# Kernel optimization log

Hardware: AMD Instinct MI355X
Metric: run time of the kernel (lower is better)

The kernel has to match this reference:

```python
import jax, jax.numpy as jnp
import numpy as np

EPS = 1e-5

def _bn(x, g, b, axes):
    # training-mode BatchNorm: biased batch stats over `axes`
    mu = jnp.mean(x, axis=axes, keepdims=True)
    var = jnp.var(x, axis=axes, keepdims=True)
    return (x - mu) * jax.lax.rsqrt(var + EPS) * g + b

def setup_inputs() -> dict:
    key = jax.random.key(0)
    ks = jax.random.split(key, 8)
    N, C, T, V = 32, 64, 512, 25
    H, D, BC = 3, 8, 16
    return {
        'x': jax.random.normal(ks[0], (N, C, T, V), jnp.float32),
        'A_topo': jax.random.uniform(ks[1], (H, V, V), jnp.float32),
        'ln_g': jnp.ones((C,), jnp.float32),
        'ln_b': jnp.zeros((C,), jnp.float32),
        'qk_w': jax.random.normal(ks[2], (2 * H * D, C), jnp.float32),
        'qk_b': jnp.zeros((2 * H * D,), jnp.float32),
        'convd_w': jax.random.normal(ks[3], (H, C, C), jnp.float32) * 0.05,
        'convd_b': jnp.zeros((H, C), jnp.float32),
        'sagc_bn_g': jnp.ones((C,), jnp.float32),
        'sagc_bn_b': jnp.zeros((C,), jnp.float32),
        'tcn_w1': jax.random.normal(ks[4], (4, BC, C), jnp.float32) * 0.1,
        'tcn_b1': jnp.zeros((4, BC), jnp.float32),
        'tcn_bn1_g': jnp.ones((4, BC), jnp.float32),
        'tcn_bn1_b': jnp.zeros((4, BC), jnp.float32),
        'tcn_w2': jax.random.normal(ks[5], (2, BC, BC, 5), jnp.float32) * 0.1,
        'tcn_b2': jnp.zeros((2, BC), jnp.float32),
        'tcn_bn2_g': jnp.ones((3, BC), jnp.float32),
        'tcn_bn2_b': jnp.zeros((3, BC), jnp.float32),
    }

def reference(x, A_topo, ln_g, ln_b, qk_w, qk_b, convd_w, convd_b,
              sagc_bn_g, sagc_bn_b, tcn_w1, tcn_b1, tcn_bn1_g, tcn_bn1_b,
              tcn_w2, tcn_b2, tcn_bn2_g, tcn_bn2_b):
    N, C, T, V = x.shape
    H = A_topo.shape[0]
    D = qk_w.shape[0] // (2 * H)
    scale = D ** -0.5

    # ---- SelfAttention ----
    feat = jnp.transpose(x, (0, 2, 3, 1))              # n t v c
    mu = feat.mean(-1, keepdims=True)
    var = feat.var(-1, keepdims=True)
    y = (feat - mu) * jax.lax.rsqrt(var + EPS) * ln_g + ln_b
    qk = y @ qk_w.T + qk_b                             # n t v 2HD
    q, k = jnp.split(qk, 2, axis=-1)
    q = q.reshape(N, T, V, H, D)
    k = k.reshape(N, T, V, H, D)
    dots = jnp.einsum('ntihd,ntjhd->nthij', q, k) * scale
    attn = jax.nn.softmax(dots, axis=-1)               # n t h v v

    # ---- SA_GC ----
    A = attn * A_topo                                  # broadcast (H,V,V)
    z = jnp.einsum('nthij,ntjc->nthic', A, feat)       # per-head A_h @ feature
    sa = jnp.einsum('nthic,hoc->noti', z, convd_w)     # fused per-head 1x1 convs
    sa = sa + convd_b.sum(0)[None, :, None, None]
    sa = _bn(sa, sagc_bn_g[None, :, None, None], sagc_bn_b[None, :, None, None], (0, 2, 3))
    y_gc = jax.nn.relu(sa + x)                         # down = identity (in==out)

    # ---- MultiScale_TemporalConv ----
    pre = jnp.einsum('nctv,koc->nkotv', y_gc, tcn_w1) + tcn_b1[None, :, :, None, None]
    pre = _bn(pre, tcn_bn1_g[None, :, :, None, None], tcn_bn1_b[None, :, :, None, None], (0, 3, 4))
    act = jax.nn.relu(pre[:, :3])                      # branches 0..2 get ReLU
    branches = []
    for i, d in enumerate((1, 2)):                     # dilated temporal convs
        pad = 2 * d                                    # (kernel-1)*d//2
        w = tcn_w2[i][:, :, :, None]                   # (O,I,5,1)
        zb = jax.lax.conv_general_dilated(
            act[:, i], w, (1, 1), ((pad, pad), (0, 0)), rhs_dilation=(d, 1),
            dimension_numbers=('NCHW', 'OIHW', 'NCHW'))
        zb = zb + tcn_b2[i][None, :, None, None]
        zb = _bn(zb, tcn_bn2_g[i][None, :, None, None], tcn_bn2_b[i][None, :, None, None], (0, 2, 3))
        branches.append(zb)
    p = jax.lax.reduce_window(act[:, 2], -jnp.inf, jax.lax.max,
                              (1, 1, 3, 1), (1, 1, 1, 1),
                              ((0, 0), (0, 0), (1, 1), (0, 0)))
    p = _bn(p, tcn_bn2_g[2][None, :, None, None], tcn_bn2_b[2][None, :, None, None], (0, 2, 3))
    branches.append(p)
    branches.append(pre[:, 3])                         # plain 1x1 branch
    tcn_out = jnp.concatenate(branches, axis=1)        # (N, C, T, V)

    # ---- EncodingBlock residual (identity: in==out, stride==1) ----
    return jax.nn.relu(tcn_out + x)
```

## Files before the change

### kernel.cpp

```cpp
#include <hip/hip_runtime.h>


#define EPS 1e-5f

typedef __bf16 bf16;
typedef __bf16 bf16x8 __attribute__((ext_vector_type(8)));
typedef float f32x4 __attribute__((ext_vector_type(4)));

__global__ void kprepack(const float* __restrict__ qk_w, const float* __restrict__ convd_w,
                         const float* __restrict__ w1g,
                         bf16* __restrict__ qkB, bf16* __restrict__ convB, bf16* __restrict__ w1B)
{
  int gid = blockIdx.x * 256 + threadIdx.x;
  if (gid < 384) {
    int lane = gid & 63, f = gid >> 6;
    int nt = f >> 1, ks = f & 1;
    int row = nt * 16 + (lane & 15);
    int col = ks * 32 + ((lane >> 4) * 8);
    const float* src = &qk_w[row * 64 + col];
    bf16* dh = &qkB[(f * 64 + lane) * 8];
    bf16* dl = dh + 3072;
    #pragma unroll
    for (int j = 0; j < 8; j++) {
      float w = src[j];
      bf16 h = (bf16)w;
      dh[j] = h;
      dl[j] = (bf16)(w - (float)h);
    }
  } else if (gid < 1920) {
    int g = gid - 384;
    int lane = g & 63, f = g >> 6;
    int nt = f / 6, ks = f - nt * 6;
    int k0 = ks * 32 + ((lane >> 4) * 8);
    int h = k0 >> 6, c = k0 & 63;
    int o = nt * 16 + (lane & 15);
    const float* src = &convd_w[(h * 64 + o) * 64 + c];
    bf16* d = &convB[(f * 64 + lane) * 8];
    #pragma unroll
    for (int j = 0; j < 8; j++) d[j] = (bf16)src[j];
  } else if (gid < 2432) {
    int g = gid - 1920;
    int lane = g & 63, f = g >> 6;
    int nt = f >> 1, ks = f & 1;
    int ko = nt * 16 + (lane & 15);
    int c0 = ks * 32 + ((lane >> 4) * 8);
    const float* src = &w1g[ko * 64 + c0];
    bf16* dh = &w1B[(f * 64 + lane) * 8];
    bf16* dl = dh + 4096;
    #pragma unroll
    for (int j = 0; j < 8; j++) {
      float w = src[j];
      bf16 h = (bf16)w;
      dh[j] = h;
      dl[j] = (bf16)(w - (float)h);
    }
  }
}

__global__ __launch_bounds__(256, 5)
void k1_sa_sagc(const float* __restrict__ x,
                const float* __restrict__ topo,
                const float* __restrict__ ln_g, const float* __restrict__ ln_b,
                const float* __restrict__ qk_b,
                const bf16* __restrict__ qkB, const bf16* __restrict__ convB,
                const float* __restrict__ convd_b,
                bf16* __restrict__ saB, float* __restrict__ pSum, float* __restrict__ pSq)
{
  const int t = blockIdx.x, n = blockIdx.y, tid = threadIdx.x;
  const int blk = n * 512 + t;
  const int lane = tid & 63, wave = tid >> 6;
  const int rr = lane & 15, co = (lane >> 4) * 8, rq = (lane >> 4) * 4;

  __shared__ __align__(16) float smem[7928];
  bf16*  featT  = (bf16*)smem;
  bf16*  yH     = (bf16*)(smem + 1280);
  bf16*  yL     = (bf16*)(smem + 2180);
  bf16*  zL     = (bf16*)(smem + 1280);
  float* sPartS = smem + 4480;
  float* sPartQ = smem + 4580;
  float* sQK    = smem + 4480;
  bf16*  sAttn  = (bf16*)(smem + 5880);
  float* sSa    = smem + 4480;
  float* sLnG   = smem + 7800;
  float* sLnB   = smem + 7864;

  const int v = tid & 31, cb = tid >> 5;
  float xv[8];
  {
    const float* xp = &x[((n * 64 + cb) * 512 + t) * 25 + (v < 25 ? v : 0)];
    float s = 0.f, q = 0.f;
    #pragma unroll
    for (int k = 0; k < 8; k++) {
      float f = (v < 25) ? xp[k * 102400] : 0.f;
      xv[k] = f;
      featT[(cb + 8 * k) * 40 + v] = (bf16)f;
      s += f; q += f * f;
    }
    s += __shfl_xor(s, 32); q += __shfl_xor(q, 32);
    if (lane < 32 && v < 25) { sPartS[v * 4 + wave] = s; sPartQ[v * 4 + wave] = q; }
    if (tid < 64) { sLnG[tid] = ln_g[tid]; sLnB[tid] = ln_b[tid]; }
  }
  __syncthreads();

  if (v < 25) {
    float S = sPartS[v * 4] + sPartS[v * 4 + 1] + sPartS[v * 4 + 2] + sPartS[v * 4 + 3];
    float Q = sPartQ[v * 4] + sPartQ[v * 4 + 1] + sPartQ[v * 4 + 2] + sPartQ[v * 4 + 3];
    float mu = S * (1.f / 64.f);
    float rstd = rsqrtf(Q * (1.f / 64.f) - mu * mu + EPS);
    #pragma unroll
    for (int k = 0; k < 8; k++) {
      int c = cb + 8 * k;
      float yv = (xv[k] - mu) * rstd * sLnG[c] + sLnB[c];
      bf16 h = (bf16)yv;
      yH[v * 72 + c] = h;
      yL[v * 72 + c] = (bf16)(yv - (float)h);
    }
  }
  __syncthreads();

  {
    const int mt = wave & 1;
    const int r0 = mt * 16 + rr;
    bf16x8 Ah[2], Al[2];
    #pragma unroll
    for (int ks = 0; ks < 2; ks++) {
      Ah[ks] = *(const bf16x8*)&yH[r0 * 72 + ks * 32 + co];
      Al[ks] = *(const bf16x8*)&yL[r0 * 72 + ks * 32 + co];
    }
    #pragma unroll
    for (int q = 0; q < 2; q++) {
      if (wave >= 2 && q > 0) break;
      int nt = (wave < 2) ? (q * 2) : 1;
      float qb = qk_b[nt * 16 + rr];
      f32x4 acc = {qb, qb, qb, qb};
      #pragma unroll
      for (int ks = 0; ks < 2; ks++) {
        bf16x8 Bh = *(const bf16x8*)&qkB[((nt * 2 + ks) * 64 + lane) * 8];
        bf16x8 Bl = *(const bf16x8*)&qkB[3072 + ((nt * 2 + ks) * 64 + lane) * 8];
        acc = __builtin_amdgcn_mfma_f32_16x16x32_bf16(Ah[ks], Bh, acc, 0, 0, 0);
        acc = __builtin_amdgcn_mfma_f32_16x16x32_bf16(Ah[ks], Bl, acc, 0, 0, 0);
        acc = __builtin_amdgcn_mfma_f32_16x16x32_bf16(Al[ks], Bh, acc, 0, 0, 0);
      }
      #pragma unroll
      for (int r = 0; r < 4; r++) {
        int i = mt * 16 + rq + r;
        if (i < 25) sQK[i * 56 + nt * 16 + rr] = acc[r];
      }
    }
  }
  __syncthreads();

  if (tid < 150) {
    int p = tid >> 1, half = tid & 1;
    int h = p / 25, i = p - (p / 25) * 25;
    const float* qr = &sQK[i * 56 + h * 8];
    float4 qa = *(const float4*)qr, qb4 = *(const float4*)(qr + 4);
    const int j0 = half * 13;
    const int cnt = 13 - half;
    float lgv[13];
    float lmax = -3.4e38f;
    #pragma unroll
    for (int jj = 0; jj < 13; jj++) {
      int j = j0 + jj; j = j > 24 ? 24 : j;
      const float* kr = &sQK[j * 56 + 24 + h * 8];
      float4 ka = *(const float4*)kr, kb = *(const float4*)(kr + 4);
      float d = qa.x * ka.x + qa.y * ka.y + qa.z * ka.z + qa.w * ka.w
              + qb4.x * kb.x + qb4.y * kb.y + qb4.z * kb.z + qb4.w * kb.w;
      d *= 0.35355339059327373f;
      lgv[jj] = d;
      lmax = fmaxf(lmax, d);
    }
    lmax = fmaxf(lmax, __shfl_xor(lmax, 1));
    float se = 0.f;
    #pragma unroll
    for (int jj = 0; jj < 13; jj++) {
      float e = __expf(lgv[jj] - lmax);
      lgv[jj] = e;
      if (jj < cnt) se += e;
    }
    se += __shfl_xor(se, 1);
    float inv = 1.f / se;
    bf16* ar = &sAttn[(h * 32 + i) * 40];
    #pragma unroll
    for (int jj = 0; jj < 13; jj++) {
      int j = j0 + jj;
      if (jj < cnt) ar[j] = (bf16)(lgv[jj] * inv * topo[(h * 25 + i) * 25 + j]);
    }
    if (half) {
      #pragma unroll
      for (int j = 25; j < 32; j++) ar[j] = (bf16)0.f;
    }
  } else if (tid >= 192 && tid < 213) {
    int k = tid - 192;
    int h = k / 7, i = 25 + (k - (k / 7) * 7);
    bf16* ar = &sAttn[(h * 32 + i) * 40];
    #pragma unroll
    for (int j = 0; j < 32; j++) ar[j] = (bf16)0.f;
  }
  __syncthreads();

  {
    const int nt = wave;
    bf16x8 Bf = *(const bf16x8*)&featT[(nt * 16 + rr) * 40 + co];
    #pragma unroll
    for (int h = 0; h < 3; h++) {
      #pragma unroll
      for (int mt = 0; mt < 2; mt++) {
        bf16x8 Af = *(const bf16x8*)&sAttn[(h * 32 + mt * 16 + rr) * 40 + co];
        f32x4 az = {0.f, 0.f, 0.f, 0.f};
        az = __builtin_amdgcn_mfma_f32_16x16x32_bf16(Af, Bf, az, 0, 0, 0);
        #pragma unroll
        for (int r = 0; r < 4; r++)
          zL[(mt * 16 + rq + r) * 200 + h * 64 + nt * 16 + rr] = (bf16)az[r];
      }
    }
  }
  __syncthreads();

  {
    const int nt = wave;
    int o = nt * 16 + rr;
    float cb2 = convd_b[o] + convd_b[64 + o] + convd_b[128 + o];
    #pragma unroll
    for (int mt = 0; mt < 2; mt++) {
      f32x4 acc = {cb2, cb2, cb2, cb2};
      #pragma unroll
      for (int ks = 0; ks < 6; ks++) {
        bf16x8 Az = *(const bf16x8*)&zL[(mt * 16 + rr) * 200 + ks * 32 + co];
        bf16x8 Bw = *(const bf16x8*)&convB[((nt * 6 + ks) * 64 + lane) * 8];
        acc = __builtin_amdgcn_mfma_f32_16x16x32_bf16(Az, Bw, acc, 0, 0, 0);
      }
      #pragma unroll
      for (int r = 0; r < 4; r++) {
        int i = mt * 16 + rq + r;
        if (i < 25) sSa[o * 29 + i] = acc[r];
      }
    }
  }
  __syncthreads();

  if (tid < 200) {
    int lin = tid * 8;
    bf16x8 s8;
    #pragma unroll
    for (int e = 0; e < 8; e++) {
      int q = lin + e, o = q / 25, i2 = q - o * 25;
      s8[e] = (bf16)sSa[o * 29 + i2];
    }
    *(bf16x8*)&saB[blk * 1600 + lin] = s8;
  }
  if (tid < 64) {
    float s = 0.f, q = 0.f;
    #pragma unroll
    for (int i = 0; i < 25; i++) { float v2 = sSa[tid * 29 + i]; s += v2; q += v2 * v2; }
    pSum[blk * 64 + tid] = s;
    pSq [blk * 64 + tid] = q;
  }
}

__global__ __launch_bounds__(256, 8)
void kpart(const float* __restrict__ pS, const float* __restrict__ pQ,
           float* __restrict__ oS, float* __restrict__ oQ)
{
  const int g = blockIdx.x, tid = threadIdx.x;
  const int c = tid & 63, r = tid >> 6;
  float s = 0.f, q = 0.f;
  for (int i = 0; i < 16; i++) {
    int b = g * 64 + r * 16 + i;
    s += pS[b * 64 + c]; q += pQ[b * 64 + c];
  }
  __shared__ float ls[4][64], lq[4][64];
  ls[r][c] = s; lq[r][c] = q;
  __syncthreads();
  if (tid < 64) {
    oS[g * 64 + tid] = ls[0][tid] + ls[1][tid] + ls[2][tid] + ls[3][tid];
    oQ[g * 64 + tid] = lq[0][tid] + lq[1][tid] + lq[2][tid] + lq[3][tid];
  }
}

__global__ __launch_bounds__(256, 4)
void kreduce(const float* __restrict__ pS, const float* __restrict__ pQ,
             int npart, int C, float invN,
             const float* __restrict__ g, const float* __restrict__ bta,
             float* __restrict__ sc, float* __restrict__ sh)
{
  int c = blockIdx.x, tid = threadIdx.x;
  float s = 0.f, q = 0.f;
  for (int i = tid; i < npart; i += 256) { s += pS[i * C + c]; q += pQ[i * C + c]; }
  #pragma unroll
  for (int m = 1; m < 64; m <<= 1) { s += __shfl_xor(s, m); q += __shfl_xor(q, m); }
  __shared__ float rs[4], rq[4];
  int w = tid >> 6;
  if ((tid & 63) == 0) { rs[w] = s; rq[w] = q; }
  __syncthreads();
  if (tid == 0) {
    float S = rs[0] + rs[1] + rs[2] + rs[3];
    float Q = rq[0] + rq[1] + rq[2] + rq[3];
    float mu = S * invN, var = Q * invN - mu * mu;
    float r = rsqrtf(var + EPS);
    sc[c] = g[c] * r;
    sh[c] = bta[c] - mu * g[c] * r;
  }
}

__global__ __launch_bounds__(256, 8)
void k3_ygc_pre(const float* __restrict__ x, const bf16* __restrict__ saB,
                const float* __restrict__ scS, const float* __restrict__ shS,
                const bf16* __restrict__ w1B, const float* __restrict__ b1,
                bf16* __restrict__ preB, float* __restrict__ pSum, float* __restrict__ pSq)
{
  const int t = blockIdx.x, n = blockIdx.y, tid = threadIdx.x;
  const int blk = n * 512 + t;
  const int lane = tid & 63, wave = tid >> 6;
  const int rr = lane & 15, co = (lane >> 4) * 8, rq = (lane >> 4) * 4;

  __shared__ __align__(16) float smem[3656];
  bf16*  yH   = (bf16*)smem;
  bf16*  yL   = (bf16*)(smem + 900);
  float* sPre = smem + 1800;

  if (tid < 200) {
    int lin = tid * 8;
    int c = lin / 25, v = lin - c * 25;
    bf16x8 s8 = *(const bf16x8*)&saB[blk * 1600 + lin];
    #pragma unroll
    for (int e = 0; e < 8; e++) {
      float val = scS[c] * (float)s8[e] + shS[c] + x[((n * 64 + c) * 512 + t) * 25 + v];
      val = fmaxf(val, 0.f);
      bf16 h = (bf16)val;
      yH[v * 72 + c] = h;
      yL[v * 72 + c] = (bf16)(val - (float)h);
      if (++v == 25) { v = 0; c++; }
    }
  }
  __syncthreads();

  {
    const int nt = wave;
    bf16x8 Ah[2][2], Al[2][2];
    #pragma unroll
    for (int mt = 0; mt < 2; mt++) {
      int r0 = mt * 16 + rr;
      #pragma unroll
      for (int ks = 0; ks < 2; ks++) {
        Ah[mt][ks] = *(const bf16x8*)&yH[r0 * 72 + ks * 32 + co];
        Al[mt][ks] = *(const bf16x8*)&yL[r0 * 72 + ks * 32 + co];
      }
    }
    float bb = b1[nt * 16 + rr];
    #pragma unroll
    for (int mt = 0; mt < 2; mt++) {
      f32x4 acc = {bb, bb, bb, bb};
      #pragma unroll
      for (int ks = 0; ks < 2; ks++) {
        bf16x8 Bh = *(const bf16x8*)&w1B[((nt * 2 + ks) * 64 + lane) * 8];
        bf16x8 Bl = *(const bf16x8*)&w1B[4096 + ((nt * 2 + ks) * 64 + lane) * 8];
        acc = __builtin_amdgcn_mfma_f32_16x16x32_bf16(Ah[mt][ks], Bh, acc, 0, 0, 0);
        acc = __builtin_amdgcn_mfma_f32_16x16x32_bf16(Ah[mt][ks], Bl, acc, 0, 0, 0);
        acc = __builtin_amdgcn_mfma_f32_16x16x32_bf16(Al[mt][ks], Bh, acc, 0, 0, 0);
      }
      #pragma unroll
      for (int r = 0; r < 4; r++) {
        int i = mt * 16 + rq + r;
        if (i < 25) sPre[(nt * 16 + rr) * 29 + i] = acc[r];
      }
    }
  }
  __syncthreads();

  if (tid < 200) {
    int lin = tid * 8;
    bf16x8 p8;
    #pragma unroll
    for (int e = 0; e < 8; e++) {
      int q = lin + e, ko = q / 25, v = q - ko * 25;
      p8[e] = (bf16)sPre[ko * 29 + v];
    }
    *(bf16x8*)&preB[blk * 1600 + lin] = p8;
  }
  if (tid < 64) {
    float s = 0.f, q = 0.f;
    #pragma unroll
    for (int i = 0; i < 25; i++) { float v = sPre[tid * 29 + i]; s += v; q += v * v; }
    pSum[blk * 64 + tid] = s;
    pSq [blk * 64 + tid] = q;
  }
}

template<int D>
__device__ __forceinline__ void conv5(const float* __restrict__ sIn, const float* __restrict__ sW,
                                      float4 bias, int o4, int v, int tb, float acc[8][4])
{
  #pragma unroll
  for (int s = 0; s < 8; s++) {
    acc[s][0] = bias.x; acc[s][1] = bias.y; acc[s][2] = bias.z; acc[s][3] = bias.w;
  }
  const int NW = 8 + 4 * D;
  for (int ic = 0; ic < 16; ic++) {
    float4 wk[5];
    #pragma unroll
    for (int kt = 0; kt < 5; kt++) wk[kt] = *(const float4*)&sW[(ic * 5 + kt) * 16 + o4];
    float xw[8 + 4 * D];
    #pragma unroll
    for (int w = 0; w < NW; w++) xw[w] = sIn[(ic * 24 + (tb - 2 * D + w + 4)) * 25 + v];
    #pragma unroll
    for (int s = 0; s < 8; s++)
      #pragma unroll
      for (int kt = 0; kt < 5; kt++) {
        float xv = xw[s + kt * D];
        acc[s][0] += xv * wk[kt].x; acc[s][1] += xv * wk[kt].y;
        acc[s][2] += xv * wk[kt].z; acc[s][3] += xv * wk[kt].w;
      }
  }
}

__global__ __launch_bounds__(256, 3)
void k5_tcn_branch(const bf16* __restrict__ preB,
                   const float* __restrict__ sc1, const float* __restrict__ sh1,
                   const float* __restrict__ w2, const float* __restrict__ b2,
                   bf16* __restrict__ zbB, float* __restrict__ pSum2, float* __restrict__ pSq2)
{
  const int tt = blockIdx.x, b = blockIdx.y, n = blockIdx.z;
  const int tid = threadIdx.x, t0 = tt * 16;
  __shared__ __align__(16) float sIn[16 * 24 * 25];
  __shared__ __align__(16) float sW[16 * 5 * 16];
  __shared__ float sRedS[4][4][4], sRedQ[4][4][4];

  for (int idx = tid; idx < 1200; idx += 256) {
    int r = idx / 50, k8 = idx - r * 50;
    int gt = t0 - 4 + r;
    int lin = k8 * 8;
    if (gt >= 0 && gt < 512) {
      bf16x8 p8 = *(const bf16x8*)&preB[((n * 512 + gt) * 64 + b * 16) * 25 + lin];
      #pragma unroll
      for (int e = 0; e < 8; e++) {
        int q = lin + e, ic = q / 25, v = q - ic * 25;
        int ch = b * 16 + ic;
        sIn[(ic * 24 + r) * 25 + v] = fmaxf(sc1[ch] * (float)p8[e] + sh1[ch], 0.f);
      }
    } else {
      #pragma unroll
      for (int e = 0; e < 8; e++) {
        int q = lin + e, ic = q / 25, v = q - ic * 25;
        sIn[(ic * 24 + r) * 25 + v] = 0.f;
      }
    }
  }
  if (b < 2)
    for (int idx = tid; idx < 1280; idx += 256) {
      int o = idx / 80, rem = idx - o * 80;
      int ic = rem / 5, kt = rem - ic * 5;
      sW[(ic * 5 + kt) * 16 + o] = w2[((b * 16 + o) * 16 + ic) * 5 + kt];
    }
  __syncthreads();

  float po[4] = {0.f, 0.f, 0.f, 0.f}, pq[4] = {0.f, 0.f, 0.f, 0.f};
  if (tid < 200) {
    int tx = tid & 3, o4 = tx * 4;
    int g = tid >> 2;
    int v = g % 25, th = g / 25;
    int tb = th * 8;
    float acc[8][4];
    if (b == 0)      conv5<1>(sIn, sW, *(const float4*)&b2[o4],      o4, v, tb, acc);
    else if (b == 1) conv5<2>(sIn, sW, *(const float4*)&b2[16 + o4], o4, v, tb, acc);
    else {
      #pragma unroll
      for (int s = 0; s < 8; s++)
        #pragma unroll
        for (int j = 0; j < 4; j++) {
          int o = o4 + j, r = tb + s + 4;
          float a = sIn[(o * 24 + r - 1) * 25 + v];
          float m = sIn[(o * 24 + r    ) * 25 + v];
          float c = sIn[(o * 24 + r + 1) * 25 + v];
          acc[s][j] = fmaxf(fmaxf(a, m), c);
        }
    }
    #pragma unroll
    for (int s = 0; s < 8; s++) {
      int gt = t0 + tb + s;
      #pragma unroll
      for (int j = 0; j < 4; j++) {
        float val = acc[s][j];
        zbB[(((b * 32 + n) * 512 + gt) * 16 + (o4 + j)) * 25 + v] = (bf16)val;
        po[j] += val; pq[j] += val * val;
      }
    }
  }
  #pragma unroll
  for (int m = 4; m < 64; m <<= 1) {
    #pragma unroll
    for (int j = 0; j < 4; j++) { po[j] += __shfl_xor(po[j], m); pq[j] += __shfl_xor(pq[j], m); }
  }
  int lane = tid & 63, w = tid >> 6;
  if (lane < 4) {
    #pragma unroll
    for (int j = 0; j < 4; j++) { sRedS[w][lane][j] = po[j]; sRedQ[w][lane][j] = pq[j]; }
  }
  __syncthreads();
  if (tid < 16) {
    int o = tid, txo = o >> 2, j = o & 3;
    float s = 0.f, q = 0.f;
    #pragma unroll
    for (int ww = 0; ww < 4; ww++) { s += sRedS[ww][txo][j]; q += sRedQ[ww][txo][j]; }
    int pidx = (n * 32 + tt) * 48 + b * 16 + o;
    pSum2[pidx] = s; pSq2[pidx] = q;
  }
}

__global__ __launch_bounds__(256, 8)
void k7_final(const float* __restrict__ x, const bf16* __restrict__ preB,
              const bf16* __restrict__ zbB,
              const float* __restrict__ sc1, const float* __restrict__ sh1,
              const float* __restrict__ sc2, const float* __restrict__ sh2,
              float* __restrict__ out)
{
  const int bid = blockIdx.x;
  const int n = bid >> 6, tc = bid & 63;
  const int t0 = tc * 8;
  for (int e = threadIdx.x; e < 12800; e += 256) {
    int ch = e / 200, r = e - ch * 200;
    int tl = r / 25, v = r - tl * 25;
    int t = t0 + tl;
    int b = ch >> 4, o = ch & 15;
    float val;
    if (b < 3) {
      val = sc2[b * 16 + o] * (float)zbB[(((b * 32 + n) * 512 + t) * 16 + o) * 25 + v]
          + sh2[b * 16 + o];
    } else {
      int ko = 48 + o;
      val = sc1[ko] * (float)preB[((n * 512 + t) * 64 + ko) * 25 + v] + sh1[ko];
    }
    int ax = (n * 64 + ch) * 12800 + t * 25 + v;
    out[ax] = fmaxf(val + x[ax], 0.f);
  }
}

extern "C" void kernel_launch(void* const* d_in, const int* in_sizes, int n_in,
                              void* d_out, int out_size, void* d_ws, size_t ws_size,
                              hipStream_t stream)
{
  const float* x       = (const float*)d_in[0];
  const float* topo    = (const float*)d_in[1];
  const float* ln_g    = (const float*)d_in[2];
  const float* ln_b    = (const float*)d_in[3];
  const float* qk_w    = (const float*)d_in[4];
  const float* qk_b    = (const float*)d_in[5];
  const float* convd_w = (const float*)d_in[6];
  const float* convd_b = (const float*)d_in[7];
  const float* sagc_g  = (const float*)d_in[8];
  const float* sagc_b  = (const float*)d_in[9];
  const float* w1      = (const float*)d_in[10];
  const float* b1      = (const float*)d_in[11];
  const float* bn1_g   = (const float*)d_in[12];
  const float* bn1_b   = (const float*)d_in[13];
  const float* w2      = (const float*)d_in[14];
  const float* b2      = (const float*)d_in[15];
  const float* bn2_g   = (const float*)d_in[16];
  const float* bn2_b   = (const float*)d_in[17];
  float* out = (float*)d_out;
  float* ws  = (float*)d_ws;

  bf16*  preB  = (bf16*)ws;
  bf16*  zbB   = (bf16*)(ws + 13107200);
  float* pSum1 = ws + 22937600;
  float* pSq1  = ws + 23986176;
  float* pSum2 = ws + 25034752;
  float* pSq2  = ws + 25083904;
  float* scS   = ws + 25133056;  float* shS = scS + 64;
  float* sc1   = scS + 128;      float* sh1 = scS + 192;
  float* sc2   = scS + 256;      float* sh2 = scS + 304;
  bf16*  qkB   = (bf16*)(ws + 25133440);
  bf16*  convB = (bf16*)(ws + 25136512);
  bf16*  w1B   = (bf16*)(ws + 25142656);
  float* oS1   = ws + 25146752;
  float* oQ1   = ws + 25163136;
  bf16*  saB   = (bf16*)d_out;

  const float invN = 1.f / 409600.f;

  kprepack<<<10, 256, 0, stream>>>(qk_w, convd_w, w1, qkB, convB, w1B);
  k1_sa_sagc<<<dim3(512, 32), 256, 0, stream>>>(x, topo, ln_g, ln_b, qk_b,
                                                qkB, convB, convd_b, saB, pSum1, pSq1);
  kpart<<<256, 256, 0, stream>>>(pSum1, pSq1, oS1, oQ1);
  kreduce<<<64, 256, 0, stream>>>(oS1, oQ1, 256, 64, invN, sagc_g, sagc_b, scS, shS);
  k3_ygc_pre<<<dim3(512, 32), 256, 0, stream>>>(x, saB, scS, shS, w1B, b1,
                                                preB, pSum1, pSq1);
  kpart<<<256, 256, 0, stream>>>(pSum1, pSq1, oS1, oQ1);
  kreduce<<<64, 256, 0, stream>>>(oS1, oQ1, 256, 64, invN, bn1_g, bn1_b, sc1, sh1);
  k5_tcn_branch<<<dim3(32, 3, 32), 256, 0, stream>>>(preB, sc1, sh1, w2, b2,
                                                     zbB, pSum2, pSq2);
  kreduce<<<48, 256, 0, stream>>>(pSum2, pSq2, 1024, 48, invN, bn2_g, bn2_b, sc2, sh2);
  k7_final<<<2048, 256, 0, stream>>>(x, preB, zbB, sc1, sh1, sc2, sh2, out);
}
```

Before: 364.2 us.

## Shrink k1 shared memory and fuse stats/store into conv epilogue for occupancy

Cuts the k1 shared-memory footprint. LN output is now stored once as fp32 and split into hi/lo bf16 at load time, the attention and z buffers are packed to 25 rows instead of padded 32, and the sSa staging buffer is removed. Occupancy hint is raised from 5 to 7 blocks per CU. The final conv epilogue writes bf16 results straight to global and reduces per-channel partial sums with shuffles, which removes one barrier and one LDS pass. In exchange, global stores are now scalar bf16 writes with a stride of 25 instead of vectorized 16-byte stores, and the overlapping aliasing of the smaller buffers needs careful padding handling.

```diff
diff --git a/kernel.cpp b/kernel.cpp
--- a/kernel.cpp
+++ b/kernel.cpp
@@ -57,7 +57,7 @@
   }
 }
 
-__global__ __launch_bounds__(256, 5)
+__global__ __launch_bounds__(256, 7)
 void k1_sa_sagc(const float* __restrict__ x,
                 const float* __restrict__ topo,
                 const float* __restrict__ ln_g, const float* __restrict__ ln_b,
@@ -71,18 +71,16 @@
   const int lane = tid & 63, wave = tid >> 6;
   const int rr = lane & 15, co = (lane >> 4) * 8, rq = (lane >> 4) * 4;
 
-  __shared__ __align__(16) float smem[7928];
+  __shared__ __align__(16) float smem[5512];
   bf16*  featT  = (bf16*)smem;
-  bf16*  yH     = (bf16*)(smem + 1280);
-  bf16*  yL     = (bf16*)(smem + 2180);
-  bf16*  zL     = (bf16*)(smem + 1280);
-  float* sPartS = smem + 4480;
-  float* sPartQ = smem + 4580;
-  float* sQK    = smem + 4480;
-  bf16*  sAttn  = (bf16*)(smem + 5880);
-  float* sSa    = smem + 4480;
-  float* sLnG   = smem + 7800;
-  float* sLnB   = smem + 7864;
+  float* yF     = smem + 1280;
+  bf16*  sAttn  = (bf16*)(smem + 1280);
+  float* sPartS = smem + 3008;
+  float* sPartQ = smem + 3208;
+  float* sLnG   = smem + 3408;
+  float* sLnB   = smem + 3472;
+  float* sQK    = smem + 3008;
+  bf16*  zL     = (bf16*)(smem + 3008);
 
   const int v = tid & 31, cb = tid >> 5;
   float xv[8];
@@ -99,6 +97,10 @@
     s += __shfl_xor(s, 32); q += __shfl_xor(q, 32);
     if (lane < 32 && v < 25) { sPartS[v * 4 + wave] = s; sPartQ[v * 4 + wave] = q; }
     if (tid < 64) { sLnG[tid] = ln_g[tid]; sLnB[tid] = ln_b[tid]; }
+    if (tid < 64) {
+      #pragma unroll
+      for (int j = 25; j < 32; j++) featT[tid * 40 + j] = (bf16)0.f;
+    }
   }
   __syncthreads();
 
@@ -110,10 +112,7 @@
     #pragma unroll
     for (int k = 0; k < 8; k++) {
       int c = cb + 8 * k;
-      float yv = (xv[k] - mu) * rstd * sLnG[c] + sLnB[c];
-      bf16 h = (bf16)yv;
-      yH[v * 72 + c] = h;
-      yL[v * 72 + c] = (bf16)(yv - (float)h);
+      yF[v * 69 + c] = (xv[k] - mu) * rstd * sLnG[c] + sLnB[c];
     }
   }
   __syncthreads();
@@ -124,8 +123,14 @@
     bf16x8 Ah[2], Al[2];
     #pragma unroll
     for (int ks = 0; ks < 2; ks++) {
-      Ah[ks] = *(const bf16x8*)&yH[r0 * 72 + ks * 32 + co];
-      Al[ks] = *(const bf16x8*)&yL[r0 * 72 + ks * 32 + co];
+      const float* yp = &yF[r0 * 69 + ks * 32 + co];
+      #pragma unroll
+      for (int j = 0; j < 8; j++) {
+        float yv = yp[j];
+        bf16 h = (bf16)yv;
+        Ah[ks][j] = h;
+        Al[ks][j] = (bf16)(yv - (float)h);
+      }
     }
     #pragma unroll
     for (int q = 0; q < 2; q++) {
@@ -180,7 +185,7 @@
     }
     se += __shfl_xor(se, 1);
     float inv = 1.f / se;
-    bf16* ar = &sAttn[(h * 32 + i) * 40];
+    bf16* ar = &sAttn[(h * 25 + i) * 40];
     #pragma unroll
     for (int jj = 0; jj < 13; jj++) {
       int j = j0 + jj;
@@ -190,12 +195,6 @@
       #pragma unroll
       for (int j = 25; j < 32; j++) ar[j] = (bf16)0.f;
     }
-  } else if (tid >= 192 && tid < 213) {
-    int k = tid - 192;
-    int h = k / 7, i = 25 + (k - (k / 7) * 7);
-    bf16* ar = &sAttn[(h * 32 + i) * 40];
-    #pragma unroll
-    for (int j = 0; j < 32; j++) ar[j] = (bf16)0.f;
   }
   __syncthreads();
 
@@ -206,12 +205,14 @@
     for (int h = 0; h < 3; h++) {
       #pragma unroll
       for (int mt = 0; mt < 2; mt++) {
-        bf16x8 Af = *(const bf16x8*)&sAttn[(h * 32 + mt * 16 + rr) * 40 + co];
+        bf16x8 Af = *(const bf16x8*)&sAttn[(h * 25 + mt * 16 + rr) * 40 + co];
         f32x4 az = {0.f, 0.f, 0.f, 0.f};
         az = __builtin_amdgcn_mfma_f32_16x16x32_bf16(Af, Bf, az, 0, 0, 0);
         #pragma unroll
-        for (int r = 0; r < 4; r++)
-          zL[(mt * 16 + rq + r) * 200 + h * 64 + nt * 16 + rr] = (bf16)az[r];
+        for (int r = 0; r < 4; r++) {
+          int i = mt * 16 + rq + r;
+          if (i < 25) zL[i * 200 + h * 64 + nt * 16 + rr] = (bf16)az[r];
+        }
       }
     }
   }
@@ -221,40 +222,34 @@
     const int nt = wave;
     int o = nt * 16 + rr;
     float cb2 = convd_b[o] + convd_b[64 + o] + convd_b[128 + o];
+    float po = 0.f, pq = 0.f;
     #pragma unroll
     for (int mt = 0; mt < 2; mt++) {
+      int zr = mt * 16 + rr;
+      zr = (zr < 25) ? zr : 0;
       f32x4 acc = {cb2, cb2, cb2, cb2};
       #pragma unroll
       for (int ks = 0; ks < 6; ks++) {
-        bf16x8 Az = *(const bf16x8*)&zL[(mt * 16 + rr) * 200 + ks * 32 + co];
+        bf16x8 Az = *(const bf16x8*)&zL[zr * 200 + ks * 32 + co];
         bf16x8 Bw = *(const bf16x8*)&convB[((nt * 6 + ks) * 64 + lane) * 8];
         acc = __builtin_amdgcn_mfma_f32_16x16x32_bf16(Az, Bw, acc, 0, 0, 0);
       }
       #pragma unroll
       for (int r = 0; r < 4; r++) {
         int i = mt * 16 + rq + r;
-        if (i < 25) sSa[o * 29 + i] = acc[r];
-      }
-    }
-  }
-  __syncthreads();
-
-  if (tid < 200) {
-    int lin = tid * 8;
-    bf16x8 s8;
-    #pragma unroll
-    for (int e = 0; e < 8; e++) {
-      int q = lin + e, o = q / 25, i2 = q - o * 25;
-      s8[e] = (bf16)sSa[o * 29 + i2];
-    }
-    *(bf16x8*)&saB[blk * 1600 + lin] = s8;
-  }
-  if (tid < 64) {
-    float s = 0.f, q = 0.f;
-    #pragma unroll
-    for (int i = 0; i < 25; i++) { float v2 = sSa[tid * 29 + i]; s += v2; q += v2 * v2; }
-    pSum[blk * 64 + tid] = s;
-    pSq [blk * 64 + tid] = q;
+        if (i < 25) {
+          float val = acc[r];
+          saB[blk * 1600 + o * 25 + i] = (bf16)val;
+          po += val; pq += val * val;
+        }
+      }
+    }
+    po += __shfl_xor(po, 16); pq += __shfl_xor(pq, 16);
+    po += __shfl_xor(po, 32); pq += __shfl_xor(pq, 32);
+    if (lane < 16) {
+      pSum[blk * 64 + o] = po;
+      pSq [blk * 64 + o] = pq;
+    }
   }
 }
 
```

Result: faster. 336.3 us (median of 3 runs) (-7.6%).
